# Kernel tuning notes

Hardware: AMD Instinct MI355X
Metric: run time of the kernel (lower is better)

Reference implementation:

```python
import jax, jax.numpy as jnp
import numpy as np
from jax import lax


def setup_inputs() -> dict:
    key = jax.random.key(0)
    k1, k2 = jax.random.split(key)
    B, E, C = 8192, 256, 25
    encodings = jax.random.normal(k1, (B, E), dtype=jnp.float32)
    categorical = jax.random.uniform(k2, (B, C), dtype=jnp.float32)
    return {"encodings": encodings, "categorical": categorical, "k": 15}


def reference(encodings, categorical, k):
    # hard cluster assignment per sample: [B]
    hard_groups = jnp.argmax(categorical, axis=1)
    n_components = categorical.shape[1]

    # pairwise Euclidean distances [B, B] via the GEMM-based cdist identity
    sq = jnp.sum(encodings * encodings, axis=1)                    # [B]
    d2 = sq[:, None] + sq[None, :] - 2.0 * (encodings @ encodings.T)
    dists = jnp.sqrt(jnp.maximum(d2, 0.0))                          # [B, B]

    # k-th smallest distance per row (tf: tf.gather(tf.sort(distances), k))
    neg_topk, _ = lax.top_k(-dists, k + 1)                          # [B, k+1]
    thresh = -neg_topk[:, k]                                        # [B]

    # strict neighbourhood mask (tf: distances < max_distance)
    mask = (dists < thresh[:, None]).astype(jnp.float32)            # [B, B]

    # per-row histogram of neighbour cluster labels via one-hot GEMM
    onehot = jax.nn.one_hot(hard_groups, n_components, dtype=jnp.float32)  # [B, C]
    counts = mask @ onehot                                          # [B, C]
    n_neigh = jnp.sum(mask, axis=1, keepdims=True)                  # [B, 1]
    bins = counts / n_neigh
    # zero-count bins contribute 0 * log(1e-5) = 0, matching tf.bincount semantics
    neighbourhood_entropy = -jnp.sum(bins * jnp.log(bins + 1e-5), axis=1)  # [B]

    # layer's call returns encodings (identity); entropy is the metric being kernel-optimized
    return encodings, neighbourhood_entropy
```

## Files before the change

### kernel.cpp

```cpp
#include <hip/hip_runtime.h>
#include <cstdint>
#include <cstring>
#include <cstddef>

#define B 8192
#define E 256
#define C 25
#define K 15

#define RB 64
#define NCHUNK 4
#define CCHUNK (B/NCHUNK)
#define CT 64
#define NTILES (CCHUNK/CT)
#define NLISTS 64
#define NREF 32

typedef short bf16x8 __attribute__((ext_vector_type(8)));
typedef float f32x16 __attribute__((ext_vector_type(16)));

union U16 { uint4 u; bf16x8 h; };

static __device__ __forceinline__ unsigned short f2bf(float f) {
    unsigned u; __builtin_memcpy(&u, &f, 4);
    u += 0x7fffu + ((u >> 16) & 1u);
    return (unsigned short)(u >> 16);
}
static __device__ __forceinline__ unsigned pack2(float a, float b) {
    return (unsigned)f2bf(a) | ((unsigned)f2bf(b) << 16);
}
static __device__ __forceinline__ unsigned umn(unsigned a, unsigned b) { return a < b ? a : b; }
static __device__ __forceinline__ unsigned umx(unsigned a, unsigned b) { return a > b ? a : b; }

static __device__ __forceinline__ void gload_lds16(const void* g, void* l) {
    __builtin_amdgcn_global_load_lds(
        (const __attribute__((address_space(1))) void*)g,
        (__attribute__((address_space(3))) void*)l, 16, 0, 0);
}

__global__ __launch_bounds__(64) void prep_kernel(
    const float* __restrict__ enc, const float* __restrict__ cat,
    float* __restrict__ out, float* __restrict__ sqg, int* __restrict__ lab,
    unsigned short* __restrict__ bfb)
{
    const int row  = blockIdx.x;
    const int lane = threadIdx.x;

    const float4 v = ((const float4*)(enc + (size_t)row * E))[lane];
    ((float4*)(out + (size_t)row * E))[lane] = v;

    uint2 p; p.x = pack2(v.x, v.y); p.y = pack2(v.z, v.w);
    ((uint2*)(bfb + (size_t)row * E))[lane] = p;

    float s = v.x * v.x + v.y * v.y + v.z * v.z + v.w * v.w;
    #pragma unroll
    for (int off = 32; off; off >>= 1) s += __shfl_xor(s, off);
    if (lane == 0) sqg[row] = s;

    float cv = (lane < C) ? cat[(size_t)row * C + lane] : -1e30f;
    int   ci = lane;
    #pragma unroll
    for (int off = 32; off; off >>= 1) {
        float ov = __shfl_xor(cv, off);
        int   oi = __shfl_xor(ci, off);
        if (ov > cv || (ov == cv && oi < ci)) { cv = ov; ci = oi; }
    }
    if (lane == 0) lab[row] = ci;
}

__global__ __launch_bounds__(256, 2) void dist_topk_kernel(
    const unsigned short* __restrict__ bfb, const float* __restrict__ sqg,
    float2* __restrict__ cand)
{
    __shared__ char smem[50176];
    uint4* lB            = (uint4*)smem;
    unsigned (*lD)[68]   = (unsigned(*)[68])(smem + 32768);
    unsigned* dumpD      = (unsigned*)smem;

    const int tid  = threadIdx.x;
    const int lane = tid & 63, wv = tid >> 6;
    const int wr = wv >> 1, wc = wv & 1;
    const int hg = lane >> 5;
    const int sr = tid >> 2, qq = tid & 3;
    const int r0 = blockIdx.x * RB;
    const int cbase = blockIdx.y * CCHUNK;

    #define STAGE_B(c0_)                                                       \
        {                                                                      \
            _Pragma("unroll")                                                  \
            for (int i = 0; i < 8; ++i) {                                      \
                const int kc = wv * 8 + i;                                     \
                const int c  = lane ^ (kc & 7);                                \
                gload_lds16(bfb + (size_t)((c0_) + c) * E + kc * 8,            \
                            (char*)smem + (size_t)kc * 1024);                  \
            }                                                                  \
        }

    bf16x8 afrag[16];
    const int arow = r0 + wr * 32 + (lane & 31);
    {
        const uint4* src = (const uint4*)(bfb + (size_t)arow * E);
        #pragma unroll
        for (int s = 0; s < 16; ++s) { U16 t; t.u = src[s * 2 + hg]; afrag[s] = t.h; }
    }
    float srw[16];
    #pragma unroll
    for (int r = 0; r < 16; ++r) {
        const int rl = wr * 32 + (r & 3) + 8 * (r >> 2) + 4 * hg;
        srw[r] = sqg[r0 + rl];
    }

    const int cl = wc * 32 + (lane & 31);
    const unsigned paylane = (unsigned)(cl & 15);

    unsigned td[16];
    #pragma unroll
    for (int i = 0; i < 16; ++i) td[i] = 0xFFFFFFFFu;

    STAGE_B(cbase);

    #pragma clang loop unroll(disable)
    for (int ct = 0; ct < NTILES; ++ct) {
        const int c0 = cbase + ct * CT;
        __syncthreads();

        const float sc = sqg[c0 + cl];

        f32x16 acc;
        #pragma unroll
        for (int i = 0; i < 16; ++i) acc[i] = 0.f;
        #pragma unroll
        for (int s = 0; s < 16; ++s) {
            const int kc = s * 2 + hg;
            U16 t; t.u = lB[kc * 64 + (cl ^ (kc & 7))];
            acc = __builtin_amdgcn_mfma_f32_32x32x16_bf16(afrag[s], t.h, acc, 0, 0, 0);
        }
        const unsigned payt = ((unsigned)ct << 4) | paylane;
        #pragma unroll
        for (int r = 0; r < 16; ++r) {
            const int rl = wr * 32 + (r & 3) + 8 * (r >> 2) + 4 * hg;
            const float d2 = fmaxf(fmaf(-2.f, acc[r], srw[r] + sc), 0.f);
            unsigned bits; __builtin_memcpy(&bits, &d2, 4);
            lD[rl][cl] = (bits & 0xFFFFFE00u) | payt;
        }
        __syncthreads();

        if (ct + 1 < NTILES) STAGE_B(c0 + CT);

        unsigned nv[16];
        {
            const uint4* rowp = (const uint4*)(&lD[sr][qq * 16]);
            #pragma unroll
            for (int q4 = 0; q4 < 4; ++q4) {
                const uint4 u = rowp[q4];
                nv[q4*4+0] = u.x; nv[q4*4+1] = u.y; nv[q4*4+2] = u.z; nv[q4*4+3] = u.w;
            }
        }
        #pragma unroll
        for (int k = 2; k <= 16; k <<= 1) {
            #pragma unroll
            for (int j = k >> 1; j > 0; j >>= 1) {
                #pragma unroll
                for (int i = 0; i < 16; ++i) {
                    const int l = i ^ j;
                    if (l > i) {
                        const unsigned a = nv[i], b = nv[l];
                        if ((i & k) == 0) { nv[i] = umn(a, b); nv[l] = umx(a, b); }
                        else             { nv[i] = umx(a, b); nv[l] = umn(a, b); }
                    }
                }
            }
        }
        unsigned m2[16];
        #pragma unroll
        for (int i = 0; i < 16; ++i) m2[i] = umn(td[i], nv[15 - i]);
        #pragma unroll
        for (int j = 8; j > 0; j >>= 1) {
            #pragma unroll
            for (int i = 0; i < 16; ++i) {
                if ((i & j) == 0) {
                    const unsigned a = m2[i], b = m2[i | j];
                    m2[i] = umn(a, b); m2[i | j] = umx(a, b);
                }
            }
        }
        #pragma unroll
        for (int i = 0; i < 16; ++i) td[i] = m2[i];
    }

    __syncthreads();
    #pragma unroll
    for (int i = 0; i < 16; ++i) dumpD[tid * 16 + i] = td[i];
    __syncthreads();

    if (tid < RB) {
        int p0 = 0, p1 = 0, p2 = 0, p3 = 0;
        const int base = tid * 4 * 16;
        float2* outp = cand + (size_t)(r0 + tid) * NLISTS + blockIdx.y * 16;
        for (int o = 0; o < 16; ++o) {
            const unsigned h0 = dumpD[base + 0*16 + p0];
            const unsigned h1 = dumpD[base + 1*16 + p1];
            const unsigned h2 = dumpD[base + 2*16 + p2];
            const unsigned h3 = dumpD[base + 3*16 + p3];
            unsigned bd = h0; int bq = 0;
            if (h1 < bd) { bd = h1; bq = 1; }
            if (h2 < bd) { bd = h2; bq = 2; }
            if (h3 < bd) { bd = h3; bq = 3; }
            const int col = cbase + (int)((bd >> 4) & 31) * CT + bq * 16 + (int)(bd & 15);
            outp[o] = make_float2(__uint_as_float(bd & 0xFFFFFE00u), __int_as_float(col));
            if (bq == 0) ++p0; else if (bq == 1) ++p1; else if (bq == 2) ++p2; else ++p3;
        }
    }
    #undef STAGE_B
}

__global__ __launch_bounds__(128) void entropy_kernel(
    const float4* __restrict__ enc4, const float2* __restrict__ cand,
    const int* __restrict__ lab, float* __restrict__ out)
{
    __shared__ float part[2][NREF][68];
    __shared__ int   colbuf[2][NREF];
    const int lane = threadIdx.x & 63;
    const int wid  = threadIdx.x >> 6;
    const int row  = blockIdx.x * 2 + wid;

    const float4 rv = enc4[(size_t)row * 64 + lane];
    const float2 cd = cand[(size_t)row * NLISTS + lane];
    const int mycol = __float_as_int(cd.y);
    unsigned mykey; __builtin_memcpy(&mykey, &cd.x, 4);

    int ar = 0;
    for (int m = 0; m < 64; ++m) {
        const unsigned km = __shfl(mykey, m);
        ar += (km < mykey || (km == mykey && m < lane)) ? 1 : 0;
    }
    if (ar < NREF) colbuf[wid][ar] = mycol;
    __syncthreads();

    #pragma unroll 4
    for (int m = 0; m < NREF; ++m) {
        const int cm = colbuf[wid][m];
        const float4 cv = enc4[(size_t)cm * 64 + lane];
        const float dx = rv.x - cv.x, dy = rv.y - cv.y;
        const float dz = rv.z - cv.z, dw = rv.w - cv.w;
        part[wid][m][lane] = dx * dx + dy * dy + dz * dz + dw * dw;
    }
    __syncthreads();

    const int ocol = colbuf[wid][lane & (NREF - 1)];
    double a = 1.0e300;
    if (lane < NREF) {
        a = 0.0;
        const float4* pr = (const float4*)&part[wid][lane][0];
        #pragma unroll
        for (int j = 0; j < 16; ++j) {
            const float4 p = pr[j];
            a += (double)p.x + (double)p.y + (double)p.z + (double)p.w;
        }
    }

    int rank = 0;
    for (int m = 0; m < 64; ++m) {
        const double dm = __shfl(a, m);
        rank += (dm < a || (dm == a && m < lane)) ? 1 : 0;
    }
    const unsigned long long b15 = __ballot(rank == K);
    const int tl = __ffsll((unsigned long long)b15) - 1;
    const double thresh = __shfl(a, tl);

    const bool act = (a < thresh);
    const int n = __popcll(__ballot(act));
    const int myval = act ? lab[ocol] : -1;

    int cnt = 0;
    for (int m = 0; m < 64; ++m) cnt += (__shfl(myval, m) == lane) ? 1 : 0;

    float H = 0.f;
    if (lane < C && n > 0) {
        const float bins = (float)cnt / (float)n;
        H = -bins * logf(bins + 1e-5f);
    }
    #pragma unroll
    for (int off = 32; off; off >>= 1) H += __shfl_xor(H, off);
    if (lane == 0) out[(size_t)B * E + row] = H;
}

extern "C" void kernel_launch(void* const* d_in, const int* in_sizes, int n_in,
                              void* d_out, int out_size, void* d_ws, size_t ws_size,
                              hipStream_t stream)
{
    (void)in_sizes; (void)n_in; (void)out_size; (void)ws_size;
    const float* enc = (const float*)d_in[0];
    const float* cat = (const float*)d_in[1];
    float*  out  = (float*)d_out;
    float*  sqg  = (float*)d_ws;
    int*    lab  = ((int*)d_ws) + B;
    float2* cand = (float2*)((char*)d_ws + (size_t)2 * B * 4);
    unsigned short* bfb =
        (unsigned short*)((char*)d_ws + (size_t)2 * B * 4 + (size_t)B * NLISTS * 8);

    prep_kernel<<<B, 64, 0, stream>>>(enc, cat, out, sqg, lab, bfb);
    dist_topk_kernel<<<dim3(B / RB, NCHUNK), 256, 0, stream>>>(bfb, sqg, cand);
    entropy_kernel<<<B / 2, 128, 0, stream>>>((const float4*)enc, cand, lab, out);
}
```

Before: 223.0 us.

## Replace bitonic per-tile sort with threshold filtering and insertion-based top-k

Result: slower. 241.8 us (+8.4%).

```diff
diff --git a/kernel.cpp b/kernel.cpp
--- a/kernel.cpp
+++ b/kernel.cpp
@@ -72,16 +72,16 @@
     const unsigned short* __restrict__ bfb, const float* __restrict__ sqg,
     float2* __restrict__ cand)
 {
-    __shared__ char smem[50176];
-    uint4* lB            = (uint4*)smem;
-    unsigned (*lD)[68]   = (unsigned(*)[68])(smem + 32768);
-    unsigned* dumpD      = (unsigned*)smem;
+    __shared__ char smem[49920];
+    uint4* lB          = (uint4*)smem;
+    unsigned* tc       = (unsigned*)(smem + 32768);
+    unsigned (*cnt)[64] = (unsigned(*)[64])(smem + 49152);
+    unsigned* thr      = (unsigned*)(smem + 49664);
 
     const int tid  = threadIdx.x;
     const int lane = tid & 63, wv = tid >> 6;
     const int wr = wv >> 1, wc = wv & 1;
     const int hg = lane >> 5;
-    const int sr = tid >> 2, qq = tid & 3;
     const int r0 = blockIdx.x * RB;
     const int cbase = blockIdx.y * CCHUNK;
 
@@ -111,20 +111,30 @@
     }
 
     const int cl = wc * 32 + (lane & 31);
-    const unsigned paylane = (unsigned)(cl & 15);
 
     unsigned td[16];
     #pragma unroll
     for (int i = 0; i < 16; ++i) td[i] = 0xFFFFFFFFu;
+    const int mrow = wv * 16 + (lane & 15);
+
+    if (tid < 64) { thr[tid] = 0xFFFFFFFFu; cnt[0][tid] = 0; cnt[1][tid] = 0; }
 
     STAGE_B(cbase);
 
     #pragma clang loop unroll(disable)
     for (int ct = 0; ct < NTILES; ++ct) {
         const int c0 = cbase + ct * CT;
+        const int par = ct & 1;
         __syncthreads();
 
         const float sc = sqg[c0 + cl];
+
+        unsigned thv[16];
+        #pragma unroll
+        for (int r = 0; r < 16; ++r) {
+            const int rl = wr * 32 + (r & 3) + 8 * (r >> 2) + 4 * hg;
+            thv[r] = thr[rl];
+        }
 
         f32x16 acc;
         #pragma unroll
@@ -135,80 +145,51 @@
             U16 t; t.u = lB[kc * 64 + (cl ^ (kc & 7))];
             acc = __builtin_amdgcn_mfma_f32_32x32x16_bf16(afrag[s], t.h, acc, 0, 0, 0);
         }
-        const unsigned payt = ((unsigned)ct << 4) | paylane;
+
+        const unsigned colbits = (unsigned)(ct * CT + cl);
         #pragma unroll
         for (int r = 0; r < 16; ++r) {
             const int rl = wr * 32 + (r & 3) + 8 * (r >> 2) + 4 * hg;
             const float d2 = fmaxf(fmaf(-2.f, acc[r], srw[r] + sc), 0.f);
             unsigned bits; __builtin_memcpy(&bits, &d2, 4);
-            lD[rl][cl] = (bits & 0xFFFFFE00u) | payt;
+            const unsigned key = (bits & 0xFFFFF800u) | colbits;
+            if (key < thv[r]) {
+                const unsigned idx = atomicAdd(&cnt[par][rl], 1u);
+                tc[idx * 64 + rl] = key;
+            }
         }
         __syncthreads();
 
         if (ct + 1 < NTILES) STAGE_B(c0 + CT);
 
-        unsigned nv[16];
-        {
-            const uint4* rowp = (const uint4*)(&lD[sr][qq * 16]);
-            #pragma unroll
-            for (int q4 = 0; q4 < 4; ++q4) {
-                const uint4 u = rowp[q4];
-                nv[q4*4+0] = u.x; nv[q4*4+1] = u.y; nv[q4*4+2] = u.z; nv[q4*4+3] = u.w;
-            }
-        }
-        #pragma unroll
-        for (int k = 2; k <= 16; k <<= 1) {
-            #pragma unroll
-            for (int j = k >> 1; j > 0; j >>= 1) {
-                #pragma unroll
-                for (int i = 0; i < 16; ++i) {
-                    const int l = i ^ j;
-                    if (l > i) {
-                        const unsigned a = nv[i], b = nv[l];
-                        if ((i & k) == 0) { nv[i] = umn(a, b); nv[l] = umx(a, b); }
-                        else             { nv[i] = umx(a, b); nv[l] = umn(a, b); }
+        if (lane < 16) {
+            const int r = mrow;
+            const int cn = (int)cnt[par][r];
+            for (int j = 0; j < cn; ++j) {
+                const unsigned x = tc[j * 64 + r];
+                if (x < td[15]) {
+                    unsigned cur = x;
+                    #pragma unroll
+                    for (int i = 0; i < 16; ++i) {
+                        const unsigned mn = umn(td[i], cur);
+                        const unsigned mx = umx(td[i], cur);
+                        td[i] = mn; cur = mx;
                     }
                 }
             }
-        }
-        unsigned m2[16];
-        #pragma unroll
-        for (int i = 0; i < 16; ++i) m2[i] = umn(td[i], nv[15 - i]);
-        #pragma unroll
-        for (int j = 8; j > 0; j >>= 1) {
-            #pragma unroll
-            for (int i = 0; i < 16; ++i) {
-                if ((i & j) == 0) {
-                    const unsigned a = m2[i], b = m2[i | j];
-                    m2[i] = umn(a, b); m2[i | j] = umx(a, b);
-                }
-            }
-        }
-        #pragma unroll
-        for (int i = 0; i < 16; ++i) td[i] = m2[i];
-    }
-
-    __syncthreads();
-    #pragma unroll
-    for (int i = 0; i < 16; ++i) dumpD[tid * 16 + i] = td[i];
-    __syncthreads();
-
-    if (tid < RB) {
-        int p0 = 0, p1 = 0, p2 = 0, p3 = 0;
-        const int base = tid * 4 * 16;
-        float2* outp = cand + (size_t)(r0 + tid) * NLISTS + blockIdx.y * 16;
+            thr[r] = td[15];
+            cnt[par ^ 1][r] = 0;
+        }
+    }
+
+    if (lane < 16) {
+        const int r = mrow;
+        float2* outp = cand + (size_t)(r0 + r) * NLISTS + blockIdx.y * 16;
+        #pragma unroll
         for (int o = 0; o < 16; ++o) {
-            const unsigned h0 = dumpD[base + 0*16 + p0];
-            const unsigned h1 = dumpD[base + 1*16 + p1];
-            const unsigned h2 = dumpD[base + 2*16 + p2];
-            const unsigned h3 = dumpD[base + 3*16 + p3];
-            unsigned bd = h0; int bq = 0;
-            if (h1 < bd) { bd = h1; bq = 1; }
-            if (h2 < bd) { bd = h2; bq = 2; }
-            if (h3 < bd) { bd = h3; bq = 3; }
-            const int col = cbase + (int)((bd >> 4) & 31) * CT + bq * 16 + (int)(bd & 15);
-            outp[o] = make_float2(__uint_as_float(bd & 0xFFFFFE00u), __int_as_float(col));
-            if (bq == 0) ++p0; else if (bq == 1) ++p1; else if (bq == 2) ++p2; else ++p3;
+            const unsigned kk = td[o];
+            outp[o] = make_float2(__uint_as_float(kk & 0xFFFFF800u),
+                                  __int_as_float(cbase + (int)(kk & 2047u)));
         }
     }
     #undef STAGE_B
```

## Keep distance tiles in registers by transposing MFMA, drop LDS transpose buffer

Applied to the files above, without the earlier changes.

Result: slower. 268.8 us (+20.5%).

```diff
diff --git a/kernel.cpp b/kernel.cpp
--- a/kernel.cpp
+++ b/kernel.cpp
@@ -68,20 +68,19 @@
     if (lane == 0) lab[row] = ci;
 }
 
-__global__ __launch_bounds__(256, 2) void dist_topk_kernel(
+__global__ __launch_bounds__(256, 4) void dist_topk_kernel(
     const unsigned short* __restrict__ bfb, const float* __restrict__ sqg,
     float2* __restrict__ cand)
 {
-    __shared__ char smem[50176];
+    __shared__ char smem[40960];
     uint4* lB            = (uint4*)smem;
-    unsigned (*lD)[68]   = (unsigned(*)[68])(smem + 32768);
-    unsigned* dumpD      = (unsigned*)smem;
+    float* scn           = (float*)(smem + 32768);
+    unsigned (*mbuf)[17] = (unsigned(*)[17])smem;
 
     const int tid  = threadIdx.x;
     const int lane = tid & 63, wv = tid >> 6;
     const int wr = wv >> 1, wc = wv & 1;
     const int hg = lane >> 5;
-    const int sr = tid >> 2, qq = tid & 3;
     const int r0 = blockIdx.x * RB;
     const int cbase = blockIdx.y * CCHUNK;
 
@@ -96,6 +95,14 @@
             }                                                                  \
         }
 
+    STAGE_B(cbase);
+
+    #pragma unroll
+    for (int i = 0; i < 8; ++i) {
+        const int ix = tid + i * 256;
+        scn[ix] = sqg[cbase + ix];
+    }
+
     bf16x8 afrag[16];
     const int arow = r0 + wr * 32 + (lane & 31);
     {
@@ -103,29 +110,19 @@
         #pragma unroll
         for (int s = 0; s < 16; ++s) { U16 t; t.u = src[s * 2 + hg]; afrag[s] = t.h; }
     }
-    float srw[16];
-    #pragma unroll
-    for (int r = 0; r < 16; ++r) {
-        const int rl = wr * 32 + (r & 3) + 8 * (r >> 2) + 4 * hg;
-        srw[r] = sqg[r0 + rl];
-    }
+    const float srw = sqg[arow];
 
     const int cl = wc * 32 + (lane & 31);
-    const unsigned paylane = (unsigned)(cl & 15);
 
     unsigned td[16];
     #pragma unroll
     for (int i = 0; i < 16; ++i) td[i] = 0xFFFFFFFFu;
-
-    STAGE_B(cbase);
 
     #pragma clang loop unroll(disable)
     for (int ct = 0; ct < NTILES; ++ct) {
         const int c0 = cbase + ct * CT;
         __syncthreads();
 
-        const float sc = sqg[c0 + cl];
-
         f32x16 acc;
         #pragma unroll
         for (int i = 0; i < 16; ++i) acc[i] = 0.f;
@@ -133,28 +130,20 @@
         for (int s = 0; s < 16; ++s) {
             const int kc = s * 2 + hg;
             U16 t; t.u = lB[kc * 64 + (cl ^ (kc & 7))];
-            acc = __builtin_amdgcn_mfma_f32_32x32x16_bf16(afrag[s], t.h, acc, 0, 0, 0);
-        }
-        const unsigned payt = ((unsigned)ct << 4) | paylane;
+            acc = __builtin_amdgcn_mfma_f32_32x32x16_bf16(t.h, afrag[s], acc, 0, 0, 0);
+        }
+        __syncthreads();
+
+        if (ct + 1 < NTILES) STAGE_B(c0 + CT);
+
+        unsigned nv[16];
         #pragma unroll
         for (int r = 0; r < 16; ++r) {
-            const int rl = wr * 32 + (r & 3) + 8 * (r >> 2) + 4 * hg;
-            const float d2 = fmaxf(fmaf(-2.f, acc[r], srw[r] + sc), 0.f);
+            const int ctile = wc * 32 + (r & 3) + 8 * (r >> 2) + 4 * hg;
+            const float sc = scn[ct * 64 + ctile];
+            const float d2 = fmaxf(fmaf(-2.f, acc[r], srw + sc), 0.f);
             unsigned bits; __builtin_memcpy(&bits, &d2, 4);
-            lD[rl][cl] = (bits & 0xFFFFFE00u) | payt;
-        }
-        __syncthreads();
-
-        if (ct + 1 < NTILES) STAGE_B(c0 + CT);
-
-        unsigned nv[16];
-        {
-            const uint4* rowp = (const uint4*)(&lD[sr][qq * 16]);
-            #pragma unroll
-            for (int q4 = 0; q4 < 4; ++q4) {
-                const uint4 u = rowp[q4];
-                nv[q4*4+0] = u.x; nv[q4*4+1] = u.y; nv[q4*4+2] = u.z; nv[q4*4+3] = u.w;
-            }
+            nv[r] = (bits & 0xFFFFF800u) | (unsigned)(ct * CT + ctile);
         }
         #pragma unroll
         for (int k = 2; k <= 16; k <<= 1) {
@@ -188,27 +177,50 @@
         for (int i = 0; i < 16; ++i) td[i] = m2[i];
     }
 
+    unsigned mt[16];
+    #pragma unroll
+    for (int i = 0; i < 16; ++i) {
+        const unsigned ov = (unsigned)__shfl_xor((int)td[15 - i], 32);
+        mt[i] = umn(td[i], ov);
+    }
+    #pragma unroll
+    for (int j = 8; j > 0; j >>= 1) {
+        #pragma unroll
+        for (int i = 0; i < 16; ++i) {
+            if ((i & j) == 0) {
+                const unsigned a = mt[i], b = mt[i | j];
+                mt[i] = umn(a, b); mt[i | j] = umx(a, b);
+            }
+        }
+    }
+
     __syncthreads();
-    #pragma unroll
-    for (int i = 0; i < 16; ++i) dumpD[tid * 16 + i] = td[i];
+    if (wc == 1 && lane < 32) {
+        #pragma unroll
+        for (int o = 0; o < 16; ++o) mbuf[wr * 32 + lane][o] = mt[o];
+    }
     __syncthreads();
-
-    if (tid < RB) {
-        int p0 = 0, p1 = 0, p2 = 0, p3 = 0;
-        const int base = tid * 4 * 16;
-        float2* outp = cand + (size_t)(r0 + tid) * NLISTS + blockIdx.y * 16;
+    if (wc == 0 && lane < 32) {
+        const int row = wr * 32 + lane;
+        unsigned fm[16];
+        #pragma unroll
+        for (int o = 0; o < 16; ++o) fm[o] = umn(mt[o], mbuf[row][15 - o]);
+        #pragma unroll
+        for (int j = 8; j > 0; j >>= 1) {
+            #pragma unroll
+            for (int i = 0; i < 16; ++i) {
+                if ((i & j) == 0) {
+                    const unsigned a = fm[i], b = fm[i | j];
+                    fm[i] = umn(a, b); fm[i | j] = umx(a, b);
+                }
+            }
+        }
+        float2* outp = cand + (size_t)(r0 + row) * NLISTS + blockIdx.y * 16;
+        #pragma unroll
         for (int o = 0; o < 16; ++o) {
-            const unsigned h0 = dumpD[base + 0*16 + p0];
-            const unsigned h1 = dumpD[base + 1*16 + p1];
-            const unsigned h2 = dumpD[base + 2*16 + p2];
-            const unsigned h3 = dumpD[base + 3*16 + p3];
-            unsigned bd = h0; int bq = 0;
-            if (h1 < bd) { bd = h1; bq = 1; }
-            if (h2 < bd) { bd = h2; bq = 2; }
-            if (h3 < bd) { bd = h3; bq = 3; }
-            const int col = cbase + (int)((bd >> 4) & 31) * CT + bq * 16 + (int)(bd & 15);
-            outp[o] = make_float2(__uint_as_float(bd & 0xFFFFFE00u), __int_as_float(col));
-            if (bq == 0) ++p0; else if (bq == 1) ++p1; else if (bq == 2) ++p2; else ++p3;
+            const unsigned kk = fm[o];
+            outp[o] = make_float2(__uint_as_float(kk & 0xFFFFF800u),
+                                  __int_as_float(cbase + (int)(kk & 2047u)));
         }
     }
     #undef STAGE_B
```
